# Optimization experiments

Hardware: AMD Instinct MI355X
Metric: run time of the kernel (lower is better)

Reference implementation:

```python
import jax, jax.numpy as jnp
import numpy as np

N_HEADS = 16
HEAD_DIM = 128
EPS = 1e-6


def _rmsnorm(t, w):
    # RMSNorm over last dim (head_dim)
    var = jnp.mean(jnp.square(t), axis=-1, keepdims=True)
    return t * jax.lax.rsqrt(var + EPS) * w


def _apply_rope(t, freqs):
    # t: [b, s, h, d]; freqs: [s, 1, d//2, 2, 2]
    b, s, h, d = t.shape
    t2 = t.reshape(b, s, h, 2, d // 2)
    t_ = jnp.moveaxis(t2, -2, -1)[..., None, :].astype(jnp.float32)  # [b,s,h,d/2,1,2]
    out = freqs[..., 0] * t_[..., 0] + freqs[..., 1] * t_[..., 1]    # [b,s,h,d/2,2]
    out = jnp.moveaxis(out, -1, -2).reshape(b, s, h, d)
    return out.astype(t.dtype)


def setup_inputs() -> dict:
    key = jax.random.key(0)
    ks = jax.random.split(key, 8)
    B, S, D = 2, 2048, 2048
    inner = N_HEADS * HEAD_DIM
    sc = 1.0 / np.sqrt(D)
    return {
        "x": jax.random.normal(ks[0], (B, S, D), jnp.float32),
        "rope_emb": jax.random.normal(ks[1], (S, 1, HEAD_DIM // 2, 2, 2), jnp.float32),
        "Wq": jax.random.normal(ks[2], (inner, D), jnp.float32) * sc,
        "Wk": jax.random.normal(ks[3], (inner, D), jnp.float32) * sc,
        "Wv": jax.random.normal(ks[4], (inner, D), jnp.float32) * sc,
        "Wo": jax.random.normal(ks[5], (D, inner), jnp.float32) * sc,
        "q_norm_w": jnp.ones((HEAD_DIM,), jnp.float32),
        "k_norm_w": jnp.ones((HEAD_DIM,), jnp.float32),
    }


def reference(x, rope_emb, Wq, Wk, Wv, Wo, q_norm_w, k_norm_w):
    b, s, _ = x.shape
    h, d = N_HEADS, HEAD_DIM
    q = (x @ Wq.T).reshape(b, s, h, d)
    k = (x @ Wk.T).reshape(b, s, h, d)
    v = (x @ Wv.T).reshape(b, s, h, d)
    q = _apply_rope(_rmsnorm(q, q_norm_w), rope_emb)
    k = _apply_rope(_rmsnorm(k, k_norm_w), rope_emb)
    # SDPA, heads-first layout
    qh = jnp.transpose(q, (0, 2, 1, 3))  # [b,h,s,d]
    kh = jnp.transpose(k, (0, 2, 1, 3))
    vh = jnp.transpose(v, (0, 2, 1, 3))
    scale = 1.0 / np.sqrt(d)
    scores = jnp.einsum('bhqd,bhkd->bhqk', qh, kh) * scale
    attn = jax.nn.softmax(scores, axis=-1)
    out = jnp.einsum('bhqk,bhkd->bhqd', attn, vh)  # [b,h,s,d]
    out = jnp.transpose(out, (0, 2, 1, 3)).reshape(b, s, h * d)
    return out @ Wo.T
```

## Files before the change

### kernel.cpp

```cpp
#include <hip/hip_runtime.h>
#include <hip/hip_bf16.h>
#include <stdint.h>

typedef __bf16 bf16;
typedef __bf16 bf16x4 __attribute__((ext_vector_type(4)));
typedef __bf16 bf16x8 __attribute__((ext_vector_type(8)));
typedef float f32x4 __attribute__((ext_vector_type(4)));
typedef float f32x16 __attribute__((ext_vector_type(16)));

#define N_HEADS 16
#define HEAD_DIM 128
#define SEQ 2048
#define DIM 2048
#define BATCH 2
#define MROWS (BATCH * SEQ)
#define NQKV (3 * DIM)
#define SM_SCALE 0.08838834764831845f
#define QSCALE_L2E 0.12751743343563824f
#define SMAX_L2E 34.624680981335122f

__device__ __forceinline__ bf16 f2b(float f) {
  union { __hip_bfloat16 h; bf16 b; } u;
  u.h = __float2bfloat16(f);
  return u.b;
}

__device__ __forceinline__ uint32_t pack2(float a, float b) {
  union { __hip_bfloat16 h; unsigned short s; } ua, ub;
  ua.h = __float2bfloat16(a); ub.h = __float2bfloat16(b);
  return (uint32_t)ua.s | ((uint32_t)ub.s << 16);
}

__device__ __forceinline__ void async16(const bf16* g, bf16* l) {
  __builtin_amdgcn_global_load_lds(
      (__attribute__((address_space(1))) void*)(uintptr_t)g,
      (__attribute__((address_space(3))) void*)(uintptr_t)l,
      16, 0, 0);
}

__global__ __launch_bounds__(256) void cvt_kernel(const float* __restrict__ src,
                                                  bf16* __restrict__ dst, int n) {
  int i = (blockIdx.x * 256 + threadIdx.x) * 8;
  if (i >= n) return;
  float4 a = *(const float4*)(src + i);
  float4 b = *(const float4*)(src + i + 4);
  bf16x8 o;
  o[0] = f2b(a.x); o[1] = f2b(a.y); o[2] = f2b(a.z); o[3] = f2b(a.w);
  o[4] = f2b(b.x); o[5] = f2b(b.y); o[6] = f2b(b.z); o[7] = f2b(b.w);
  *(bf16x8*)(dst + i) = o;
}

__global__ __launch_bounds__(256) void cvt_w4(const float* __restrict__ w0,
                                              const float* __restrict__ w1,
                                              const float* __restrict__ w2,
                                              const float* __restrict__ w3,
                                              bf16* __restrict__ wqkv,
                                              bf16* __restrict__ wo) {
  const int per = (DIM * DIM) / 8 / 256;
  int which = blockIdx.x / per;
  int i = (blockIdx.x % per) * 256 * 8 + threadIdx.x * 8;
  const float* src = which == 0 ? w0 : which == 1 ? w1 : which == 2 ? w2 : w3;
  bf16* dst = which < 3 ? wqkv + (size_t)which * DIM * DIM : wo;
  float4 a = *(const float4*)(src + i);
  float4 b = *(const float4*)(src + i + 4);
  bf16x8 o;
  o[0] = f2b(a.x); o[1] = f2b(a.y); o[2] = f2b(a.z); o[3] = f2b(a.w);
  o[4] = f2b(b.x); o[5] = f2b(b.y); o[6] = f2b(b.z); o[7] = f2b(b.w);
  *(bf16x8*)(dst + i) = o;
}

__device__ __forceinline__ void gemm_tile_mainloop(
    const bf16* __restrict__ A, const bf16* __restrict__ Bw, int K,
    int rowBase, int colBase, bf16* lA, bf16* lB, f32x4 acc[4][4]) {
  const int t = threadIdx.x;
  const int w = t >> 6, lane = t & 63;
  const int lm = lane & 15, quad = lane >> 4;
  const int wr = (w >> 1) * 64, wc = (w & 1) * 64;

  for (int kt = 0; kt < K; kt += 32) {
#pragma unroll
    for (int i = 0; i < 2; i++) {
      const int c = i * 256 + t;
      const int r = c >> 2, cc = (c & 3) << 3;
      async16(A + (size_t)(rowBase + r) * K + (kt + cc), lA + (i * 256 + w * 64) * 8);
      async16(Bw + (size_t)(colBase + r) * K + (kt + cc), lB + (i * 256 + w * 64) * 8);
    }
    asm volatile("s_waitcnt vmcnt(0)" ::: "memory");
    __syncthreads();
    bf16x8 af[4], bfr[4];
#pragma unroll
    for (int f = 0; f < 4; f++)
      af[f] = *(const bf16x8*)(lA + (wr + f * 16 + lm) * 32 + quad * 8);
#pragma unroll
    for (int f = 0; f < 4; f++)
      bfr[f] = *(const bf16x8*)(lB + (wc + f * 16 + lm) * 32 + quad * 8);
#pragma unroll
    for (int fr = 0; fr < 4; fr++)
#pragma unroll
      for (int fc = 0; fc < 4; fc++)
        acc[fr][fc] = __builtin_amdgcn_mfma_f32_16x16x32_bf16(af[fr], bfr[fc], acc[fr][fc], 0, 0, 0);
    __syncthreads();
  }
}

__global__ __launch_bounds__(256) void gemm_qkv(const bf16* __restrict__ X,
                                                const bf16* __restrict__ W,
                                                bf16* __restrict__ Q,
                                                bf16* __restrict__ Kv,
                                                bf16* __restrict__ VT) {
  __shared__ __align__(16) bf16 lA[128 * 32];
  __shared__ __align__(16) bf16 lB[128 * 32];
  f32x4 acc[4][4];
  f32x4 z = {0.f, 0.f, 0.f, 0.f};
#pragma unroll
  for (int i = 0; i < 4; i++)
#pragma unroll
    for (int j = 0; j < 4; j++) acc[i][j] = z;

  const int rowBase = blockIdx.y * 128, colBase = blockIdx.x * 128;
  gemm_tile_mainloop(X, W, DIM, rowBase, colBase, lA, lB, acc);

  const int t = threadIdx.x, w = t >> 6, lane = t & 63;
  const int lm = lane & 15, quad = lane >> 4;
  const int wr = (w >> 1) * 64, wc = (w & 1) * 64;
  const int which = colBase >> 11;
  if (which < 2) {
    bf16* dst = which ? Kv : Q;
#pragma unroll
    for (int fr = 0; fr < 4; fr++)
#pragma unroll
      for (int fc = 0; fc < 4; fc++)
#pragma unroll
        for (int r = 0; r < 4; r++) {
          int m = rowBase + wr + fr * 16 + quad * 4 + r;
          int n = (colBase + wc + fc * 16 + lm) & 2047;
          int h = n >> 7, d = n & 127;
          int b = m >> 11, s = m & 2047;
          dst[(((size_t)(b * N_HEADS + h) * SEQ) + s) * HEAD_DIM + d] = f2b(acc[fr][fc][r]);
        }
  } else {
#pragma unroll
    for (int fr = 0; fr < 4; fr++)
#pragma unroll
      for (int fc = 0; fc < 4; fc++) {
        int n = (colBase + wc + fc * 16 + lm) & 2047;
        int h = n >> 7, d = n & 127;
        int m = rowBase + wr + fr * 16 + quad * 4;
        int b = m >> 11, s = m & 2047;
        bf16x4 pk;
#pragma unroll
        for (int r = 0; r < 4; r++) pk[r] = f2b(acc[fr][fc][r]);
        *(bf16x4*)&VT[((size_t)(b * N_HEADS + h) * HEAD_DIM + d) * SEQ + s] = pk;
      }
  }
}

__global__ __launch_bounds__(256) void gemm_out(const bf16* __restrict__ A,
                                                const bf16* __restrict__ W,
                                                float* __restrict__ out) {
  __shared__ __align__(16) bf16 lA[128 * 32];
  __shared__ __align__(16) bf16 lB[128 * 32];
  f32x4 acc[4][4];
  f32x4 z = {0.f, 0.f, 0.f, 0.f};
#pragma unroll
  for (int i = 0; i < 4; i++)
#pragma unroll
    for (int j = 0; j < 4; j++) acc[i][j] = z;

  const int rowBase = blockIdx.y * 128, colBase = blockIdx.x * 128;
  gemm_tile_mainloop(A, W, DIM, rowBase, colBase, lA, lB, acc);

  const int t = threadIdx.x, w = t >> 6, lane = t & 63;
  const int lm = lane & 15, quad = lane >> 4;
  const int wr = (w >> 1) * 64, wc = (w & 1) * 64;
#pragma unroll
  for (int fr = 0; fr < 4; fr++)
#pragma unroll
    for (int fc = 0; fc < 4; fc++)
#pragma unroll
      for (int r = 0; r < 4; r++) {
        int m = rowBase + wr + fr * 16 + quad * 4 + r;
        int n = colBase + wc + fc * 16 + lm;
        out[(size_t)m * DIM + n] = acc[fr][fc][r];
      }
}

__global__ __launch_bounds__(256) void norm_rope(bf16* __restrict__ Q,
                                                 bf16* __restrict__ K,
                                                 const float* __restrict__ rope,
                                                 const float* __restrict__ qw,
                                                 const float* __restrict__ kw) {
  const int t = threadIdx.x, w = t >> 6, lane = t & 63;
  const int rid = blockIdx.x * 4 + w;
  const int which = rid >> 16;
  const int row = rid & 65535;
  bf16* ptr = (which ? K : Q) + (size_t)row * HEAD_DIM;
  const float* nw = which ? kw : qw;
  const int s = row & (SEQ - 1);

  float x0 = (float)ptr[lane];
  float x1 = (float)ptr[lane + 64];
  float ss = x0 * x0 + x1 * x1;
#pragma unroll
  for (int off = 32; off; off >>= 1) ss += __shfl_xor(ss, off);
  float r = rsqrtf(ss * (1.f / 128.f) + 1e-6f);
  float x0n = x0 * r * nw[lane];
  float x1n = x1 * r * nw[lane + 64];
  float4 f = ((const float4*)rope)[s * 64 + lane];
  float y0 = f.x * x0n + f.y * x1n;
  float y1 = f.z * x0n + f.w * x1n;
  if (!which) { y0 *= QSCALE_L2E; y1 *= QSCALE_L2E; }
  ptr[lane] = f2b(y0);
  ptr[lane + 64] = f2b(y1);
}

__global__ __launch_bounds__(256, 2) void attn_kernel(const bf16* __restrict__ Q,
                                                      const bf16* __restrict__ K,
                                                      const bf16* __restrict__ VT,
                                                      bf16* __restrict__ O) {
  __shared__ __align__(16) bf16 Ks[128 * 128];
  __shared__ __align__(16) bf16 Vs[128 * 128];

  const int t = threadIdx.x, w = t >> 6, lane = t & 63;
  const int lq = lane & 31, h = lane >> 5;
  const int bh = blockIdx.x, qt = blockIdx.y;

  bf16x8 qf[8];
  {
    const bf16* Qp = Q + ((size_t)bh * SEQ + qt * 128 + w * 32 + lq) * HEAD_DIM;
#pragma unroll
    for (int ks = 0; ks < 8; ks++)
      qf[ks] = *(const bf16x8*)(Qp + ks * 16 + h * 8);
  }

  f32x16 oacc[4];
#pragma unroll
  for (int nb = 0; nb < 4; nb++)
#pragma unroll
    for (int e = 0; e < 16; e++) oacc[nb][e] = 0.f;
  float rsum = 0.f;

  const bf16* kbase = K + (size_t)bh * SEQ * HEAD_DIM;
  const bf16* vbase = VT + (size_t)bh * HEAD_DIM * SEQ;

  const int srow = w * 32 + (lane >> 4), scc = lane & 15;
  bf16x8 kreg[8], vreg[8];

  auto load_tile = [&](int j) {
    const bf16* kp = kbase + (size_t)j * 128 * HEAD_DIM;
    const bf16* vp = vbase + j * 128;
#pragma unroll
    for (int i = 0; i < 8; i++)
      kreg[i] = *(const bf16x8*)(kp + (size_t)(srow + i * 4) * HEAD_DIM + scc * 8);
#pragma unroll
    for (int i = 0; i < 8; i++)
      vreg[i] = *(const bf16x8*)(vp + (size_t)(srow + i * 4) * SEQ + scc * 8);
  };

  load_tile(0);

  for (int j = 0; j < SEQ / 128; j++) {
#pragma unroll
    for (int i = 0; i < 8; i++) {
      int r = srow + i * 4;
      *(bf16x8*)&Ks[r * 128 + ((scc ^ (r & 15)) << 3)] = kreg[i];
    }
#pragma unroll
    for (int i = 0; i < 8; i++) {
      int d = srow + i * 4;
      *(bf16x8*)&Vs[d * 128 + ((scc ^ (d & 15)) << 3)] = vreg[i];
    }
    __syncthreads();

    if (j + 1 < SEQ / 128) load_tile(j + 1);

#pragma unroll
    for (int bp = 0; bp < 2; bp++) {
      f32x16 sacc[2];
#pragma unroll
      for (int bb = 0; bb < 2; bb++)
#pragma unroll
        for (int e = 0; e < 16; e++) sacc[bb][e] = -SMAX_L2E;
      const int r0 = bp * 64 + lq, r1 = r0 + 32;
#pragma unroll
      for (int ks = 0; ks < 8; ks++) {
        int c = ks * 2 + h;
        bf16x8 kf0 = *(const bf16x8*)&Ks[r0 * 128 + ((c ^ (r0 & 15)) << 3)];
        bf16x8 kf1 = *(const bf16x8*)&Ks[r1 * 128 + ((c ^ (r1 & 15)) << 3)];
        sacc[0] = __builtin_amdgcn_mfma_f32_32x32x16_bf16(kf0, qf[ks], sacc[0], 0, 0, 0);
        sacc[1] = __builtin_amdgcn_mfma_f32_32x32x16_bf16(kf1, qf[ks], sacc[1], 0, 0, 0);
      }

      uint32_t a1[2][4], a2[2][4];
#pragma unroll
      for (int bb = 0; bb < 2; bb++) {
        float e[16];
        float p0 = 0.f, p1 = 0.f, p2 = 0.f, p3 = 0.f;
#pragma unroll
        for (int r = 0; r < 16; r += 4) {
          e[r]     = __builtin_amdgcn_exp2f(sacc[bb][r]);
          e[r + 1] = __builtin_amdgcn_exp2f(sacc[bb][r + 1]);
          e[r + 2] = __builtin_amdgcn_exp2f(sacc[bb][r + 2]);
          e[r + 3] = __builtin_amdgcn_exp2f(sacc[bb][r + 3]);
          p0 += e[r]; p1 += e[r + 1]; p2 += e[r + 2]; p3 += e[r + 3];
        }
        rsum += (p0 + p1) + (p2 + p3);
        uint32_t pk[8];
#pragma unroll
        for (int i = 0; i < 8; i++) pk[i] = pack2(e[2 * i], e[2 * i + 1]);
        uint32_t ta = h ? pk[0] : pk[2], tb = h ? pk[1] : pk[3];
        uint32_t tc = h ? pk[4] : pk[6], td = h ? pk[5] : pk[7];
        uint32_t ra = __shfl_xor((int)ta, 32), rb = __shfl_xor((int)tb, 32);
        uint32_t rc = __shfl_xor((int)tc, 32), rd = __shfl_xor((int)td, 32);
        a1[bb][0] = h ? ra : pk[0]; a1[bb][1] = h ? rb : pk[1];
        a1[bb][2] = h ? pk[2] : ra; a1[bb][3] = h ? pk[3] : rb;
        a2[bb][0] = h ? rc : pk[4]; a2[bb][1] = h ? rd : pk[5];
        a2[bb][2] = h ? pk[6] : rc; a2[bb][3] = h ? pk[7] : rd;
      }

#pragma unroll
      for (int bb = 0; bb < 2; bb++)
#pragma unroll
        for (int ks2 = 0; ks2 < 2; ks2++) {
          union { uint32_t u[4]; bf16x8 v; } ap;
#pragma unroll
          for (int i = 0; i < 4; i++) ap.u[i] = ks2 ? a2[bb][i] : a1[bb][i];
          int c2 = (bp * 2 + bb) * 4 + ks2 * 2 + h;
#pragma unroll
          for (int nb = 0; nb < 4; nb++) {
            int rv = nb * 32 + lq;
            bf16x8 bv = *(const bf16x8*)&Vs[rv * 128 + ((c2 ^ (rv & 15)) << 3)];
            oacc[nb] = __builtin_amdgcn_mfma_f32_32x32x16_bf16(ap.v, bv, oacc[nb], 0, 0, 0);
          }
        }
    }
    __syncthreads();
  }

  rsum += __shfl_xor(rsum, 32);
  float inv = 1.f / rsum;
  const int b = bh >> 4, hh = bh & 15;
#pragma unroll
  for (int nb = 0; nb < 4; nb++)
#pragma unroll
    for (int r = 0; r < 16; r++) {
      int q = (r & 3) + 8 * (r >> 2) + 4 * h;
      float iv = __shfl(inv, q);
      int qg = qt * 128 + w * 32 + q;
      O[((size_t)b * SEQ + qg) * DIM + hh * HEAD_DIM + nb * 32 + lq] = f2b(oacc[nb][r] * iv);
    }
}

extern "C" void kernel_launch(void* const* d_in, const int* in_sizes, int n_in,
                              void* d_out, int out_size, void* d_ws, size_t ws_size,
                              hipStream_t stream) {
  const float* x    = (const float*)d_in[0];
  const float* rope = (const float*)d_in[1];
  const float* Wq   = (const float*)d_in[2];
  const float* Wk   = (const float*)d_in[3];
  const float* Wv   = (const float*)d_in[4];
  const float* Wo   = (const float*)d_in[5];
  const float* qw   = (const float*)d_in[6];
  const float* kw   = (const float*)d_in[7];
  float* out = (float*)d_out;

  char* ws = (char*)d_ws;
  bf16* xb   = (bf16*)ws;
  bf16* wqkv = (bf16*)(ws + (16u << 20));
  bf16* wo   = (bf16*)(ws + (40u << 20));
  bf16* qb   = (bf16*)(ws + (48u << 20));
  bf16* kb   = (bf16*)(ws + (64u << 20));
  bf16* vt   = (bf16*)(ws + (80u << 20));
  bf16* attn = xb;

  const int NX = MROWS * DIM;
  const int NW = DIM * DIM;

  cvt_kernel<<<NX / 8 / 256, 256, 0, stream>>>(x, xb, NX);
  cvt_w4<<<4 * (NW / 8 / 256), 256, 0, stream>>>(Wq, Wk, Wv, Wo, wqkv, wo);

  gemm_qkv<<<dim3(NQKV / 128, MROWS / 128), 256, 0, stream>>>(xb, wqkv, qb, kb, vt);
  norm_rope<<<(2 * BATCH * N_HEADS * SEQ) / 4, 256, 0, stream>>>(qb, kb, rope, qw, kw);
  attn_kernel<<<dim3(BATCH * N_HEADS, SEQ / 128), 256, 0, stream>>>(qb, kb, vt, attn);
  gemm_out<<<dim3(DIM / 128, MROWS / 128), 256, 0, stream>>>(attn, wo, out);
}
```

Baseline: 417.7 us.

## Rewrite QKV GEMM with 256x256 tiles, double-buffered async LDS pipeline

Replaces the 128x128 QKV projection GEMM with a 512-thread 256x256-tile kernel. It uses K=64 double-buffered LDS stages with XOR-swizzled layout, interleaves async global-to-LDS loads with MFMA phases under barriers and setprio, and remaps block ids for L2 locality. The aim is to raise arithmetic intensity and hide global load latency, which the old single-buffered loop exposed. The cost is 128KB of LDS per block, a large accumulator register set, and a complex hand-tuned barrier schedule that is fragile to get right.

```diff
diff --git a/kernel.cpp b/kernel.cpp
--- a/kernel.cpp
+++ b/kernel.cpp
@@ -18,6 +18,8 @@
 #define SM_SCALE 0.08838834764831845f
 #define QSCALE_L2E 0.12751743343563824f
 #define SMAX_L2E 34.624680981335122f
+
+#define MFMA16(a, b, c) __builtin_amdgcn_mfma_f32_16x16x32_bf16(a, b, c, 0, 0, 0)
 
 __device__ __forceinline__ bf16 f2b(float f) {
   union { __hip_bfloat16 h; bf16 b; } u;
@@ -69,6 +71,188 @@
   *(bf16x8*)(dst + i) = o;
 }
 
+
+#define GBAR() asm volatile("s_barrier" ::: "memory")
+#define GWAITL() do { asm volatile("s_waitcnt lgkmcnt(0)" ::: "memory"); \
+                      __builtin_amdgcn_sched_barrier(0); } while (0)
+
+__device__ __forceinline__ void g256_stage_half(const bf16* gbase, bf16* lbase,
+                                                int w, int lane, int t, int hf) {
+  const int kt = t * 64;
+#pragma unroll
+  for (int i = 0; i < 2; i++) {
+    const int rbase = hf * 128 + w * 16 + i * 8;
+    const int r = rbase + (lane >> 3);
+    async16(gbase + (size_t)r * 2048 + kt + 8 * ((lane & 7) ^ (r & 7)),
+            lbase + rbase * 64);
+  }
+}
+
+__device__ __forceinline__ void g256_lda(const bf16* lbase, int wm, int lm,
+                                         int quad, int mh, bf16x8 a[4][2]) {
+#pragma unroll
+  for (int f = 0; f < 4; f++) {
+    const int row = wm * 128 + mh * 64 + f * 16 + lm;
+    const char* p = (const char*)lbase + row * 128;
+    const int sw = (row & 7) << 4;
+#pragma unroll
+    for (int s = 0; s < 2; s++)
+      a[f][s] = *(const bf16x8*)(p + ((s * 64 + quad * 16) ^ sw));
+  }
+}
+
+__device__ __forceinline__ void g256_ldb(const bf16* lbase, int wn, int lm,
+                                         int quad, int nh, bf16x8 bb[2][2]) {
+#pragma unroll
+  for (int g = 0; g < 2; g++) {
+    const int row = wn * 64 + nh * 32 + g * 16 + lm;
+    const char* p = (const char*)lbase + row * 128;
+    const int sw = (row & 7) << 4;
+#pragma unroll
+    for (int s = 0; s < 2; s++)
+      bb[g][s] = *(const bf16x8*)(p + ((s * 64 + quad * 16) ^ sw));
+  }
+}
+
+__device__ __forceinline__ void g256_mma(f32x4 acc[8][4], bf16x8 a[4][2],
+                                         bf16x8 bb[2][2], int mh, int nh) {
+  __builtin_amdgcn_s_setprio(1);
+#pragma unroll
+  for (int s = 0; s < 2; s++)
+#pragma unroll
+    for (int f = 0; f < 4; f++)
+#pragma unroll
+      for (int g = 0; g < 2; g++)
+        acc[mh * 4 + f][nh * 2 + g] =
+            MFMA16(a[f][s], bb[g][s], acc[mh * 4 + f][nh * 2 + g]);
+  __builtin_amdgcn_s_setprio(0);
+}
+
+__device__ __forceinline__ void gemm256_mainloop(
+    const bf16* __restrict__ Ag, const bf16* __restrict__ Bg,
+    bf16* sA0, bf16* sA1, bf16* sB0, bf16* sB1, f32x4 acc[8][4],
+    int w, int lane, int wm, int wn, int lm, int quad) {
+  g256_stage_half(Ag, sA0, w, lane, 0, 0);
+  g256_stage_half(Ag, sA0, w, lane, 0, 1);
+  g256_stage_half(Bg, sB0, w, lane, 0, 0);
+  g256_stage_half(Bg, sB0, w, lane, 0, 1);
+  g256_stage_half(Ag, sA1, w, lane, 1, 0);
+  g256_stage_half(Ag, sA1, w, lane, 1, 1);
+  asm volatile("s_waitcnt vmcnt(0)" ::: "memory");
+  GBAR();
+
+  bf16x8 a0[4][2], a1[4][2], bb[2][2];
+
+  for (int i = 0; i < 16; i++) {
+    const int t1 = 2 * i + 1;
+    const int t2 = t1 + 1 < 32 ? t1 + 1 : 31;
+    const int t3 = t1 + 2 < 32 ? t1 + 2 : 31;
+    g256_lda(sA0, wm, lm, quad, 0, a0);
+    g256_ldb(sB0, wn, lm, quad, 0, bb);
+    g256_stage_half(Bg, sB1, w, lane, t1, 0);
+    GBAR(); GWAITL();
+    g256_mma(acc, a0, bb, 0, 0);
+    GBAR();
+    g256_lda(sA0, wm, lm, quad, 1, a1);
+    g256_stage_half(Bg, sB1, w, lane, t1, 1);
+    GBAR(); GWAITL();
+    g256_mma(acc, a1, bb, 1, 0);
+    GBAR();
+    g256_ldb(sB0, wn, lm, quad, 1, bb);
+    g256_stage_half(Ag, sA0, w, lane, t2, 0);
+    GBAR(); GWAITL();
+    g256_mma(acc, a1, bb, 1, 1);
+    GBAR();
+    g256_stage_half(Ag, sA0, w, lane, t2, 1);
+    asm volatile("s_waitcnt vmcnt(4)" ::: "memory");
+    GBAR(); GWAITL();
+    g256_mma(acc, a0, bb, 0, 1);
+    GBAR();
+    g256_lda(sA1, wm, lm, quad, 0, a0);
+    g256_ldb(sB1, wn, lm, quad, 0, bb);
+    g256_stage_half(Bg, sB0, w, lane, t2, 0);
+    GBAR(); GWAITL();
+    g256_mma(acc, a0, bb, 0, 0);
+    GBAR();
+    g256_lda(sA1, wm, lm, quad, 1, a1);
+    g256_stage_half(Bg, sB0, w, lane, t2, 1);
+    GBAR(); GWAITL();
+    g256_mma(acc, a1, bb, 1, 0);
+    GBAR();
+    g256_ldb(sB1, wn, lm, quad, 1, bb);
+    g256_stage_half(Ag, sA1, w, lane, t3, 0);
+    GBAR(); GWAITL();
+    g256_mma(acc, a1, bb, 1, 1);
+    GBAR();
+    g256_stage_half(Ag, sA1, w, lane, t3, 1);
+    asm volatile("s_waitcnt vmcnt(4)" ::: "memory");
+    GBAR(); GWAITL();
+    g256_mma(acc, a0, bb, 0, 1);
+    GBAR();
+  }
+  asm volatile("s_waitcnt vmcnt(0)" ::: "memory");
+}
+
+__global__ __launch_bounds__(512, 2) void gemm_qkv(const bf16* __restrict__ X,
+                                                   const bf16* __restrict__ W,
+                                                   bf16* __restrict__ Q,
+                                                   bf16* __restrict__ Kv,
+                                                   bf16* __restrict__ VT) {
+  __shared__ __align__(16) bf16 sA[2][256 * 64];
+  __shared__ __align__(16) bf16 sB[2][256 * 64];
+  const int t = threadIdx.x, w = t >> 6, lane = t & 63;
+  const int lm = lane & 15, quad = lane >> 4;
+  const int wm = w >> 2, wn = w & 3;
+  const int bid = blockIdx.x;
+  const int swz = (bid & 7) * 48 + (bid >> 3);
+  const int bm = swz / 24, bn = swz % 24;
+  const int rowBase = bm * 256, colBase = bn * 256;
+
+  f32x4 acc[8][4];
+  f32x4 z = {0.f, 0.f, 0.f, 0.f};
+#pragma unroll
+  for (int i = 0; i < 8; i++)
+#pragma unroll
+    for (int j = 0; j < 4; j++) acc[i][j] = z;
+
+  gemm256_mainloop(X + (size_t)rowBase * 2048, W + (size_t)colBase * 2048,
+                   sA[0], sA[1], sB[0], sB[1], acc, w, lane, wm, wn, lm, quad);
+
+  const int which = colBase >> 11;
+  if (which < 2) {
+    bf16* dst = which ? Kv : Q;
+#pragma unroll
+    for (int fi = 0; fi < 8; fi++)
+#pragma unroll
+      for (int gj = 0; gj < 4; gj++) {
+        const int mb = rowBase + wm * 128 + fi * 16 + quad * 4;
+        const int nc = (colBase + wn * 64 + gj * 16 + lm) & 2047;
+        const int hh = nc >> 7, d = nc & 127;
+#pragma unroll
+        for (int r = 0; r < 4; r++) {
+          const int m = mb + r;
+          const int b = m >> 11, s = m & 2047;
+          dst[(((size_t)(b * N_HEADS + hh) * SEQ) + s) * HEAD_DIM + d] =
+              f2b(acc[fi][gj][r]);
+        }
+      }
+  } else {
+#pragma unroll
+    for (int fi = 0; fi < 8; fi++)
+#pragma unroll
+      for (int gj = 0; gj < 4; gj++) {
+        const int mb = rowBase + wm * 128 + fi * 16 + quad * 4;
+        const int nc = (colBase + wn * 64 + gj * 16 + lm) & 2047;
+        const int hh = nc >> 7, d = nc & 127;
+        const int b = mb >> 11, s = mb & 2047;
+        bf16x4 pk;
+#pragma unroll
+        for (int r = 0; r < 4; r++) pk[r] = f2b(acc[fi][gj][r]);
+        *(bf16x4*)&VT[((size_t)(b * N_HEADS + hh) * HEAD_DIM + d) * SEQ + s] = pk;
+      }
+  }
+}
+
 __device__ __forceinline__ void gemm_tile_mainloop(
     const bf16* __restrict__ A, const bf16* __restrict__ Bw, int K,
     int rowBase, int colBase, bf16* lA, bf16* lB, f32x4 acc[4][4]) {
@@ -98,60 +282,8 @@
     for (int fr = 0; fr < 4; fr++)
 #pragma unroll
       for (int fc = 0; fc < 4; fc++)
-        acc[fr][fc] = __builtin_amdgcn_mfma_f32_16x16x32_bf16(af[fr], bfr[fc], acc[fr][fc], 0, 0, 0);
+        acc[fr][fc] = MFMA16(af[fr], bfr[fc], acc[fr][fc]);
     __syncthreads();
-  }
-}
-
-__global__ __launch_bounds__(256) void gemm_qkv(const bf16* __restrict__ X,
-                                                const bf16* __restrict__ W,
-                                                bf16* __restrict__ Q,
-                                                bf16* __restrict__ Kv,
-                                                bf16* __restrict__ VT) {
-  __shared__ __align__(16) bf16 lA[128 * 32];
-  __shared__ __align__(16) bf16 lB[128 * 32];
-  f32x4 acc[4][4];
-  f32x4 z = {0.f, 0.f, 0.f, 0.f};
-#pragma unroll
-  for (int i = 0; i < 4; i++)
-#pragma unroll
-    for (int j = 0; j < 4; j++) acc[i][j] = z;
-
-  const int rowBase = blockIdx.y * 128, colBase = blockIdx.x * 128;
-  gemm_tile_mainloop(X, W, DIM, rowBase, colBase, lA, lB, acc);
-
-  const int t = threadIdx.x, w = t >> 6, lane = t & 63;
-  const int lm = lane & 15, quad = lane >> 4;
-  const int wr = (w >> 1) * 64, wc = (w & 1) * 64;
-  const int which = colBase >> 11;
-  if (which < 2) {
-    bf16* dst = which ? Kv : Q;
-#pragma unroll
-    for (int fr = 0; fr < 4; fr++)
-#pragma unroll
-      for (int fc = 0; fc < 4; fc++)
-#pragma unroll
-        for (int r = 0; r < 4; r++) {
-          int m = rowBase + wr + fr * 16 + quad * 4 + r;
-          int n = (colBase + wc + fc * 16 + lm) & 2047;
-          int h = n >> 7, d = n & 127;
-          int b = m >> 11, s = m & 2047;
-          dst[(((size_t)(b * N_HEADS + h) * SEQ) + s) * HEAD_DIM + d] = f2b(acc[fr][fc][r]);
-        }
-  } else {
-#pragma unroll
-    for (int fr = 0; fr < 4; fr++)
-#pragma unroll
-      for (int fc = 0; fc < 4; fc++) {
-        int n = (colBase + wc + fc * 16 + lm) & 2047;
-        int h = n >> 7, d = n & 127;
-        int m = rowBase + wr + fr * 16 + quad * 4;
-        int b = m >> 11, s = m & 2047;
-        bf16x4 pk;
-#pragma unroll
-        for (int r = 0; r < 4; r++) pk[r] = f2b(acc[fr][fc][r]);
-        *(bf16x4*)&VT[((size_t)(b * N_HEADS + h) * HEAD_DIM + d) * SEQ + s] = pk;
-      }
   }
 }
 
@@ -379,7 +511,7 @@
   cvt_kernel<<<NX / 8 / 256, 256, 0, stream>>>(x, xb, NX);
   cvt_w4<<<4 * (NW / 8 / 256), 256, 0, stream>>>(Wq, Wk, Wv, Wo, wqkv, wo);
 
-  gemm_qkv<<<dim3(NQKV / 128, MROWS / 128), 256, 0, stream>>>(xb, wqkv, qb, kb, vt);
+  gemm_qkv<<<(MROWS / 256) * (NQKV / 256), 512, 0, stream>>>(xb, wqkv, qb, kb, vt);
   norm_rope<<<(2 * BATCH * N_HEADS * SEQ) / 4, 256, 0, stream>>>(qb, kb, rope, qw, kw);
   attn_kernel<<<dim3(BATCH * N_HEADS, SEQ / 128), 256, 0, stream>>>(qb, kb, vt, attn);
   gemm_out<<<dim3(DIM / 128, MROWS / 128), 256, 0, stream>>>(attn, wo, out);
```

Measured after the change: 416.3 us. About the same (-0.3%).
